# Kernel optimization log

Hardware: AMD Instinct MI355X
Metric: run time of the kernel (lower is better)

## Reference

```python
import jax, jax.numpy as jnp
import numpy as np

P = 65536          # collocation points
J = 16             # num_subdomains == pou num_partitions
WID = 64           # subnet width_size
N_SUB_HID = 2      # subnet depth=3 -> 2 extra hidden linear layers after the input layer
H = 64             # pou hidden_dim
N_POU_RES = 4      # pou depth=6 -> 4 residual blocks


def setup_inputs() -> dict:
    key = jax.random.key(0)
    ks = jax.random.split(key, 14)
    s = 0.1  # small init scale for stable tanh/softmax
    return {
        "x": jax.random.uniform(ks[0], (P, 2), jnp.float32),
        "sub_W0": s * jax.random.normal(ks[1], (J, 2, WID), jnp.float32),
        "sub_b0": s * jax.random.normal(ks[2], (J, WID), jnp.float32),
        "sub_Wh": s * jax.random.normal(ks[3], (J, N_SUB_HID, WID, WID), jnp.float32),
        "sub_bh": s * jax.random.normal(ks[4], (J, N_SUB_HID, WID), jnp.float32),
        "sub_Wl": s * jax.random.normal(ks[5], (J, WID, 1), jnp.float32),
        "sub_bl": s * jax.random.normal(ks[6], (J, 1), jnp.float32),
        "pou_W0": s * jax.random.normal(ks[7], (2, H), jnp.float32),
        "pou_b0": s * jax.random.normal(ks[8], (H,), jnp.float32),
        "pou_Wh": s * jax.random.normal(ks[9], (N_POU_RES, H, H), jnp.float32),
        "pou_bh": s * jax.random.normal(ks[10], (N_POU_RES, H), jnp.float32),
        "pou_Wl": s * jax.random.normal(ks[11], (H, J), jnp.float32),
        "pou_bl": s * jax.random.normal(ks[12], (J,), jnp.float32),
    }


def reference(x, sub_W0, sub_b0, sub_Wh, sub_bh, sub_Wl, sub_bl,
              pou_W0, pou_b0, pou_Wh, pou_bh, pou_Wl, pou_bl):
    x = jnp.atleast_2d(x)
    # --- ResPOUNet2D.forward: partition-of-unity weights (computed ONCE, not per j) ---
    h = jax.nn.relu(x @ pou_W0 + pou_b0)                      # [P, H]
    for i in range(pou_Wh.shape[0]):                          # residual relu blocks
        h = h + jax.nn.relu(h @ pou_Wh[i] + pou_bh[i])
    w_all = jax.nn.softmax(h @ pou_Wl + pou_bl, axis=-1)      # [P, J]
    # --- batched subnets: eqx.nn.MLP with tanh, applied to (x-0.5)*2 ---
    xs = (x - 0.5) * 2.0                                      # [P, 2]
    hs = jnp.tanh(jnp.einsum('pd,jdw->jpw', xs, sub_W0) + sub_b0[:, None, :])  # [J, P, W]
    for i in range(sub_Wh.shape[1]):
        hs = jnp.tanh(jnp.einsum('jpw,jwv->jpv', hs, sub_Wh[:, i]) + sub_bh[:, i][:, None, :])
    u = (jnp.einsum('jpw,jwo->jpo', hs, sub_Wl) + sub_bl[:, None, :])[..., 0]  # [J, P]
    # --- weighted sum over subdomains ---
    total = jnp.einsum('pj,jp->p', w_all, u)                  # [P]
    # --- ansatz: hard zero-Dirichlet BC on unit square ---
    return total * jnp.sin(jnp.pi * x[:, 0]) * jnp.sin(jnp.pi * x[:, 1])
```

## Files before the change

kernel.cpp:

```cpp
#include <hip/hip_runtime.h>
#include <math.h>

#define NP 65536
#define NJ 16
#define WID 64
#define HH 64
#define NPOU 4
#define NSUB 2
#define L2E2 2.8853900817779268f

typedef __attribute__((ext_vector_type(8))) short short8;
typedef __attribute__((ext_vector_type(4))) float f32x4;
typedef __attribute__((ext_vector_type(4))) int int4v;

#define CHUNK_US(row, chunk) ((((row) << 6)) + ((((chunk) ^ ((row) & 7))) << 3))
__device__ __forceinline__ int usIdx(int row, int col) {
    return ((row) << 6) + ((((col >> 3) ^ (row & 7))) << 3) + (col & 7);
}

__device__ __forceinline__ unsigned short f2bf(float f) {
    unsigned u = __float_as_uint(f);
    u += 0x7FFFu + ((u >> 16) & 1u);
    return (unsigned short)(u >> 16);
}
__device__ __forceinline__ unsigned short rhu(float f) {
    return (unsigned short)((__float_as_uint(f) + 0x8000u) >> 16);
}
__device__ __forceinline__ unsigned pk2(float a, float b) {
    unsigned ua = __float_as_uint(a) + 0x8000u;
    unsigned ub = __float_as_uint(b) + 0x8000u;
    return __builtin_amdgcn_perm(ub, ua, 0x07060302u);
}
__device__ __forceinline__ unsigned cvtpk(float a, float b) {
    unsigned r;
    asm("v_cvt_pk_bf16_f32 %0, %1, %2" : "=v"(r) : "v"(a), "v"(b));
    return r;
}
__device__ __forceinline__ float bf2f(unsigned short s) {
    return __uint_as_float(((unsigned)s) << 16);
}
__device__ __forceinline__ float tanh2(float y) {
    float e = __builtin_amdgcn_exp2f(y);
    return fmaf(-2.0f, __builtin_amdgcn_rcpf(e + 1.0f), 1.0f);
}
__device__ __forceinline__ short8 mk8(unsigned a, unsigned b, unsigned c, unsigned d) {
    int4v t; t.x = (int)a; t.y = (int)b; t.z = (int)c; t.w = (int)d;
    return __builtin_bit_cast(short8, t);
}

__global__ __launch_bounds__(256) void pou_mfma_kernel(
    const float* __restrict__ x,
    const float* __restrict__ W0, const float* __restrict__ b0,
    const float* __restrict__ Wh, const float* __restrict__ bh,
    const float* __restrict__ Wl, const float* __restrict__ bl,
    float* __restrict__ w_all)
{
    __shared__ unsigned short sA[4 * 64 * 64];
    __shared__ unsigned short sWhT[NPOU * 64 * 64];
    __shared__ unsigned short sWlT[16 * 64];
    __shared__ float sW0a[HH], sW0b[HH], sB0[HH];
    __shared__ float sbh[NPOU * HH];
    __shared__ float sbl[NJ];

    const int tid  = threadIdx.x;
    const int wave = tid >> 6;
    const int lane = tid & 63;
    const int r15  = lane & 15;
    const int g    = lane >> 4;

    for (int idx = tid; idx < NPOU * HH * HH; idx += 256) {
        int r = idx >> 12, k = (idx >> 6) & 63, n = idx & 63;
        sWhT[r * 4096 + usIdx(n, k)] = f2bf(Wh[idx]);
    }
    for (int idx = tid; idx < HH * NJ; idx += 256) {
        int k = idx >> 4, j = idx & 15;
        sWlT[usIdx(j, k)] = f2bf(Wl[idx]);
    }
    if (tid < HH) { sW0a[tid] = W0[tid]; sW0b[tid] = W0[HH + tid]; sB0[tid] = b0[tid]; }
    for (int i = tid; i < NPOU * HH; i += 256) sbh[i] = bh[i];
    if (tid < NJ) sbl[tid] = bl[tid];
    __syncthreads();

    unsigned short* myA = &sA[wave * 4096];
    const int pbase = blockIdx.x * 256;

    {
        const int p = pbase + tid;
        float2 xv = ((const float2*)x)[p];
        float v[HH];
#pragma unroll
        for (int c = 0; c < HH; ++c)
            v[c] = fmaxf(fmaf(xv.x, sW0a[c], fmaf(xv.y, sW0b[c], sB0[c])), 0.0f);
#pragma unroll
        for (int c = 0; c < 8; ++c) {
            int4v r;
            r.x = (int)pk2(v[8 * c + 0], v[8 * c + 1]);
            r.y = (int)pk2(v[8 * c + 2], v[8 * c + 3]);
            r.z = (int)pk2(v[8 * c + 4], v[8 * c + 5]);
            r.w = (int)pk2(v[8 * c + 6], v[8 * c + 7]);
            *(int4v*)&myA[CHUNK_US(lane, c)] = r;
        }
    }

    float trunk[4][4][4];
#pragma unroll
    for (int mt = 0; mt < 4; ++mt)
#pragma unroll
        for (int nt = 0; nt < 4; ++nt)
#pragma unroll
            for (int q = 0; q < 4; ++q)
                trunk[mt][nt][q] = bf2f(myA[usIdx(mt * 16 + g * 4 + q, nt * 16 + r15)]);

#pragma unroll 1
    for (int r = 0; r < NPOU; ++r) {
        const unsigned short* wt = &sWhT[r * 4096];
        short8 bfr[2][4];
#pragma unroll
        for (int kc = 0; kc < 2; ++kc)
#pragma unroll
            for (int nt = 0; nt < 4; ++nt)
                bfr[kc][nt] = *(const short8*)&wt[CHUNK_US(nt * 16 + r15, kc * 4 + g)];
        float bias[4];
#pragma unroll
        for (int nt = 0; nt < 4; ++nt) bias[nt] = sbh[r * HH + nt * 16 + r15];

#pragma unroll
        for (int mt = 0; mt < 4; ++mt) {
            short8 a0 = *(const short8*)&myA[CHUNK_US(mt * 16 + r15, g)];
            short8 a1 = *(const short8*)&myA[CHUNK_US(mt * 16 + r15, 4 + g)];
            f32x4 acc[4];
#pragma unroll
            for (int nt = 0; nt < 4; ++nt) {
                acc[nt] = (f32x4)(0.0f);
                acc[nt] = __builtin_amdgcn_mfma_f32_16x16x32_bf16(a0, bfr[0][nt], acc[nt], 0, 0, 0);
                acc[nt] = __builtin_amdgcn_mfma_f32_16x16x32_bf16(a1, bfr[1][nt], acc[nt], 0, 0, 0);
            }
#pragma unroll
            for (int nt = 0; nt < 4; ++nt)
#pragma unroll
                for (int q = 0; q < 4; ++q) {
                    float t = trunk[mt][nt][q] + fmaxf(acc[nt][q] + bias[nt], 0.0f);
                    trunk[mt][nt][q] = t;
                    myA[usIdx(mt * 16 + g * 4 + q, nt * 16 + r15)] = rhu(t);
                }
        }
    }

    short8 bw0 = *(const short8*)&sWlT[CHUNK_US(r15, g)];
    short8 bw1 = *(const short8*)&sWlT[CHUNK_US(r15, 4 + g)];
    float lg[4][4], mx[4][4];
#pragma unroll
    for (int mt = 0; mt < 4; ++mt) {
        short8 a0 = *(const short8*)&myA[CHUNK_US(mt * 16 + r15, g)];
        short8 a1 = *(const short8*)&myA[CHUNK_US(mt * 16 + r15, 4 + g)];
        f32x4 acc = (f32x4)(0.0f);
        acc = __builtin_amdgcn_mfma_f32_16x16x32_bf16(a0, bw0, acc, 0, 0, 0);
        acc = __builtin_amdgcn_mfma_f32_16x16x32_bf16(a1, bw1, acc, 0, 0, 0);
#pragma unroll
        for (int q = 0; q < 4; ++q) { lg[mt][q] = acc[q] + sbl[r15]; mx[mt][q] = lg[mt][q]; }
    }
#pragma unroll
    for (int mask = 1; mask < 16; mask <<= 1)
#pragma unroll
        for (int mt = 0; mt < 4; ++mt)
#pragma unroll
            for (int q = 0; q < 4; ++q) mx[mt][q] = fmaxf(mx[mt][q], __shfl_xor(mx[mt][q], mask));
    float ev[4][4], sm[4][4];
#pragma unroll
    for (int mt = 0; mt < 4; ++mt)
#pragma unroll
        for (int q = 0; q < 4; ++q) { ev[mt][q] = __expf(lg[mt][q] - mx[mt][q]); sm[mt][q] = ev[mt][q]; }
#pragma unroll
    for (int mask = 1; mask < 16; mask <<= 1)
#pragma unroll
        for (int mt = 0; mt < 4; ++mt)
#pragma unroll
            for (int q = 0; q < 4; ++q) sm[mt][q] += __shfl_xor(sm[mt][q], mask);
#pragma unroll
    for (int mt = 0; mt < 4; ++mt)
#pragma unroll
        for (int q = 0; q < 4; ++q) {
            const int p = pbase + wave * 64 + mt * 16 + g * 4 + q;
            w_all[r15 * NP + p] = ev[mt][q] * __builtin_amdgcn_rcpf(sm[mt][q]);
        }
}

__global__ __launch_bounds__(256) void prep_kernel(
    const float* __restrict__ gW0, const float* __restrict__ gb0,
    const float* __restrict__ gWh, const float* __restrict__ gbh,
    const float* __restrict__ gWl, const float* __restrict__ gbl,
    int4v* __restrict__ wfrag, float* __restrict__ prm)
{
    const int j   = blockIdx.y;
    const int tid = threadIdx.x;
    const int f   = blockIdx.x * 256 + tid;
    const int lane = f & 63, kc = (f >> 6) & 1, mt = (f >> 7) & 3, L = f >> 9;
    const int c = lane & 15, g = lane >> 4;
    const int n = mt * 16 + c;

    const float* src = gWh + j * (NSUB * WID * WID) + L * 4096;
    unsigned w[4];
#pragma unroll
    for (int e2 = 0; e2 < 4; ++e2) {
        int k = kc * 32 + 8 * g + 2 * e2;
        float v0 = L2E2 * src[k * 64 + n];
        float v1 = L2E2 * src[(k + 1) * 64 + n];
        w[e2] = (unsigned)f2bf(v0) | ((unsigned)f2bf(v1) << 16);
    }
    int4v r; r.x = (int)w[0]; r.y = (int)w[1]; r.z = (int)w[2]; r.w = (int)w[3];
    wfrag[j * 1024 + f] = r;

    if (blockIdx.x == 0) {
        float* pj = prm + j * 512;
        if (tid < WID) {
            float w0 = gW0[j * 2 * WID + tid], w1 = gW0[j * 2 * WID + WID + tid];
            pj[tid]       = 2.0f * L2E2 * w0;
            pj[64 + tid]  = 2.0f * L2E2 * w1;
            pj[128 + tid] = L2E2 * (gb0[j * WID + tid] - w0 - w1);
        }
        if (tid < NSUB * WID) pj[192 + tid] = L2E2 * gbh[j * NSUB * WID + tid];
        if (tid < WID) pj[320 + tid] = gWl[j * WID + tid];
        if (tid == 0) pj[384] = gbl[j];
    }
}

__global__ __launch_bounds__(256, 4) void subnet_nolds_kernel(
    const float* __restrict__ x,
    const short8* __restrict__ wfrag,
    const float* __restrict__ prm,
    const float* __restrict__ w_all,
    float* __restrict__ upart)
{
    const int tid  = threadIdx.x;
    const int j    = blockIdx.y;
    const int wave = tid >> 6;
    const int lane = tid & 63;
    const int c    = lane & 15;
    const int g    = lane >> 4;

    const float*  pj = prm + j * 512;
    const short8* wf = wfrag + j * 1024;
    const int pb = blockIdx.x * 256 + wave * 64;

    short8 bf[2][4];
    {
        float xs0[4], xs1[4];
#pragma unroll
        for (int nt = 0; nt < 4; ++nt) {
            float2 xv = ((const float2*)x)[pb + nt * 16 + c];
            xs0[nt] = xv.x; xs1[nt] = xv.y;
        }
        f32x4 wa[2][2], wb[2][2], bb[2][2];
#pragma unroll
        for (int kc = 0; kc < 2; ++kc)
#pragma unroll
            for (int hf = 0; hf < 2; ++hf) {
                wa[kc][hf] = *(const f32x4*)&pj[      kc * 32 + 8 * g + 4 * hf];
                wb[kc][hf] = *(const f32x4*)&pj[ 64 + kc * 32 + 8 * g + 4 * hf];
                bb[kc][hf] = *(const f32x4*)&pj[128 + kc * 32 + 8 * g + 4 * hf];
            }
        unsigned t[2][4][4];
#pragma unroll
        for (int kc = 0; kc < 2; ++kc)
#pragma unroll
            for (int pr = 0; pr < 4; ++pr) {
                const int h0 = pr >> 1, e0 = (2 * pr) & 3, e1 = e0 + 1;
#pragma unroll
                for (int nt = 0; nt < 4; ++nt) {
                    float v0 = tanh2(fmaf(xs0[nt], wa[kc][h0][e0], fmaf(xs1[nt], wb[kc][h0][e0], bb[kc][h0][e0])));
                    float v1 = tanh2(fmaf(xs0[nt], wa[kc][h0][e1], fmaf(xs1[nt], wb[kc][h0][e1], bb[kc][h0][e1])));
                    t[kc][nt][pr] = cvtpk(v0, v1);
                }
            }
#pragma unroll
        for (int kc = 0; kc < 2; ++kc)
#pragma unroll
            for (int nt = 0; nt < 4; ++nt)
                bf[kc][nt] = mk8(t[kc][nt][0], t[kc][nt][1], t[kc][nt][2], t[kc][nt][3]);
    }

    float red[4];
#pragma unroll
    for (int nt = 0; nt < 4; ++nt) red[nt] = 0.0f;

#pragma unroll
    for (int L = 0; L < NSUB; ++L) {
        short8 aw[4][2];
#pragma unroll
        for (int mt = 0; mt < 4; ++mt)
#pragma unroll
            for (int kc = 0; kc < 2; ++kc)
                aw[mt][kc] = wf[((L * 4 + mt) * 2 + kc) * 64 + lane];
        f32x4 bias[4];
#pragma unroll
        for (int mt = 0; mt < 4; ++mt)
            bias[mt] = *(const f32x4*)&pj[192 + L * 64 + mt * 16 + 4 * g];

#pragma unroll
        for (int nt = 0; nt < 4; ++nt) {
            f32x4 acc[4];
#pragma unroll
            for (int mt = 0; mt < 4; ++mt) acc[mt] = bias[mt];
#pragma unroll
            for (int mt = 0; mt < 4; ++mt) {
                acc[mt] = __builtin_amdgcn_mfma_f32_16x16x32_bf16(aw[mt][0], bf[0][nt], acc[mt], 0, 0, 0);
                acc[mt] = __builtin_amdgcn_mfma_f32_16x16x32_bf16(aw[mt][1], bf[1][nt], acc[mt], 0, 0, 0);
            }

            if (L < NSUB - 1) {
                float h[4][4];
#pragma unroll
                for (int mt = 0; mt < 4; ++mt)
#pragma unroll
                    for (int q = 0; q < 4; ++q) h[mt][q] = tanh2(acc[mt][q]);
#pragma unroll
                for (int kn = 0; kn < 2; ++kn) {
                    unsigned A0 = cvtpk(h[2 * kn][0],     h[2 * kn][1]);
                    unsigned A1 = cvtpk(h[2 * kn][2],     h[2 * kn][3]);
                    unsigned B0 = cvtpk(h[2 * kn + 1][0], h[2 * kn + 1][1]);
                    unsigned B1 = cvtpk(h[2 * kn + 1][2], h[2 * kn + 1][3]);
                    asm("v_permlane32_swap_b32 %0, %1" : "+v"(A0), "+v"(B0));
                    asm("v_permlane16_swap_b32 %0, %1" : "+v"(A0), "+v"(B0));
                    asm("v_permlane32_swap_b32 %0, %1" : "+v"(A1), "+v"(B1));
                    asm("v_permlane16_swap_b32 %0, %1" : "+v"(A1), "+v"(B1));
                    bf[kn][nt] = mk8(A0, A1, B0, B1);
                }
            } else {
#pragma unroll
                for (int mt = 0; mt < 4; ++mt) {
                    f32x4 wlv = *(const f32x4*)&pj[320 + mt * 16 + 4 * g];
#pragma unroll
                    for (int q = 0; q < 4; ++q)
                        red[nt] = fmaf(tanh2(acc[mt][q]), wlv[q], red[nt]);
                }
            }
        }
    }

#pragma unroll
    for (int nt = 0; nt < 4; ++nt) {
        red[nt] += __shfl_xor(red[nt], 16);
        red[nt] += __shfl_xor(red[nt], 32);
    }
    float u = (g & 1) ? ((g & 2) ? red[3] : red[1]) : ((g & 2) ? red[2] : red[0]);
    u += pj[384];

    const int p = pb + lane;
    upart[j * NP + p] = u * w_all[j * NP + p];
}

__global__ __launch_bounds__(256) void subnet_mfma_fallback(
    const float* __restrict__ x,
    const float* __restrict__ gW0, const float* __restrict__ gb0,
    const float* __restrict__ gWh, const float* __restrict__ gbh,
    const float* __restrict__ gWl, const float* __restrict__ gbl,
    const float* __restrict__ w_all,
    float* __restrict__ upart)
{
    __shared__ __align__(16) unsigned short sWt[NSUB * 64 * 64];
    __shared__ __align__(16) float sW0a[WID], sW0b[WID], sB0[WID];
    __shared__ __align__(16) float sbh[NSUB * WID];
    __shared__ __align__(16) float sWl[WID];
    __shared__ float sbl1v;

    const int tid  = threadIdx.x;
    const int j    = blockIdx.y;
    const int wave = tid >> 6;
    const int lane = tid & 63;
    const int c    = lane & 15;
    const int g    = lane >> 4;

    {
        const float* src = gWh + j * (NSUB * WID * WID);
        for (int idx = tid; idx < NSUB * WID * WID; idx += 256) {
            int L = idx >> 12, rem = idx & 4095;
            int k = rem >> 6, n = rem & 63;
            sWt[L * 4096 + usIdx(n, k)] = f2bf(L2E2 * src[idx]);
        }
        if (tid < WID) {
            float w0 = gW0[j * 2 * WID + tid], w1 = gW0[j * 2 * WID + WID + tid];
            sW0a[tid] = 2.0f * L2E2 * w0;
            sW0b[tid] = 2.0f * L2E2 * w1;
            sB0[tid]  = L2E2 * (gb0[j * WID + tid] - w0 - w1);
        }
        if (tid < NSUB * WID) sbh[tid] = L2E2 * gbh[j * NSUB * WID + tid];
        if (tid < WID) sWl[tid] = gWl[j * WID + tid];
        if (tid == 0) sbl1v = gbl[j];
    }
    __syncthreads();

    const int pb = blockIdx.x * 256 + wave * 64;

    short8 bf[2][4];
    {
        float xs0[4], xs1[4];
#pragma unroll
        for (int nt = 0; nt < 4; ++nt) {
            float2 xv = ((const float2*)x)[pb + nt * 16 + c];
            xs0[nt] = xv.x; xs1[nt] = xv.y;
        }
        f32x4 wa[2][2], wb[2][2], bb[2][2];
#pragma unroll
        for (int kc = 0; kc < 2; ++kc)
#pragma unroll
            for (int hf = 0; hf < 2; ++hf) {
                wa[kc][hf] = *(const f32x4*)&sW0a[kc * 32 + 8 * g + 4 * hf];
                wb[kc][hf] = *(const f32x4*)&sW0b[kc * 32 + 8 * g + 4 * hf];
                bb[kc][hf] = *(const f32x4*)&sB0 [kc * 32 + 8 * g + 4 * hf];
            }
        unsigned t[2][4][4];
#pragma unroll
        for (int kc = 0; kc < 2; ++kc)
#pragma unroll
            for (int pr = 0; pr < 4; ++pr) {
                const int h0 = pr >> 1, e0 = (2 * pr) & 3, e1 = e0 + 1;
#pragma unroll
                for (int nt = 0; nt < 4; ++nt) {
                    float v0 = tanh2(fmaf(xs0[nt], wa[kc][h0][e0], fmaf(xs1[nt], wb[kc][h0][e0], bb[kc][h0][e0])));
                    float v1 = tanh2(fmaf(xs0[nt], wa[kc][h0][e1], fmaf(xs1[nt], wb[kc][h0][e1], bb[kc][h0][e1])));
                    t[kc][nt][pr] = cvtpk(v0, v1);
                }
            }
#pragma unroll
        for (int kc = 0; kc < 2; ++kc)
#pragma unroll
            for (int nt = 0; nt < 4; ++nt)
                bf[kc][nt] = mk8(t[kc][nt][0], t[kc][nt][1], t[kc][nt][2], t[kc][nt][3]);
    }

    float red[4];
#pragma unroll
    for (int nt = 0; nt < 4; ++nt) red[nt] = 0.0f;

#pragma unroll
    for (int L = 0; L < NSUB; ++L) {
        const unsigned short* wt = &sWt[L * 4096];
        short8 aw[4][2];
#pragma unroll
        for (int mt = 0; mt < 4; ++mt)
#pragma unroll
            for (int kc = 0; kc < 2; ++kc)
                aw[mt][kc] = *(const short8*)&wt[CHUNK_US(mt * 16 + c, kc * 4 + g)];
        f32x4 bias[4];
#pragma unroll
        for (int mt = 0; mt < 4; ++mt)
            bias[mt] = *(const f32x4*)&sbh[L * 64 + mt * 16 + 4 * g];

#pragma unroll
        for (int nt = 0; nt < 4; ++nt) {
            f32x4 acc[4];
#pragma unroll
            for (int mt = 0; mt < 4; ++mt) acc[mt] = bias[mt];
#pragma unroll
            for (int mt = 0; mt < 4; ++mt) {
                acc[mt] = __builtin_amdgcn_mfma_f32_16x16x32_bf16(aw[mt][0], bf[0][nt], acc[mt], 0, 0, 0);
                acc[mt] = __builtin_amdgcn_mfma_f32_16x16x32_bf16(aw[mt][1], bf[1][nt], acc[mt], 0, 0, 0);
            }

            if (L < NSUB - 1) {
                float h[4][4];
#pragma unroll
                for (int mt = 0; mt < 4; ++mt)
#pragma unroll
                    for (int q = 0; q < 4; ++q) h[mt][q] = tanh2(acc[mt][q]);
#pragma unroll
                for (int kn = 0; kn < 2; ++kn) {
                    unsigned A0 = cvtpk(h[2 * kn][0],     h[2 * kn][1]);
                    unsigned A1 = cvtpk(h[2 * kn][2],     h[2 * kn][3]);
                    unsigned B0 = cvtpk(h[2 * kn + 1][0], h[2 * kn + 1][1]);
                    unsigned B1 = cvtpk(h[2 * kn + 1][2], h[2 * kn + 1][3]);
                    asm("v_permlane32_swap_b32 %0, %1" : "+v"(A0), "+v"(B0));
                    asm("v_permlane16_swap_b32 %0, %1" : "+v"(A0), "+v"(B0));
                    asm("v_permlane32_swap_b32 %0, %1" : "+v"(A1), "+v"(B1));
                    asm("v_permlane16_swap_b32 %0, %1" : "+v"(A1), "+v"(B1));
                    bf[kn][nt] = mk8(A0, A1, B0, B1);
                }
            } else {
#pragma unroll
                for (int mt = 0; mt < 4; ++mt) {
                    f32x4 wlv = *(const f32x4*)&sWl[mt * 16 + 4 * g];
#pragma unroll
                    for (int q = 0; q < 4; ++q)
                        red[nt] = fmaf(tanh2(acc[mt][q]), wlv[q], red[nt]);
                }
            }
        }
    }

#pragma unroll
    for (int nt = 0; nt < 4; ++nt) {
        red[nt] += __shfl_xor(red[nt], 16);
        red[nt] += __shfl_xor(red[nt], 32);
    }
    float u = (g & 1) ? ((g & 2) ? red[3] : red[1]) : ((g & 2) ? red[2] : red[0]);
    u += sbl1v;

    const int p = pb + lane;
    upart[j * NP + p] = u * w_all[j * NP + p];
}

__global__ __launch_bounds__(256) void reduce_kernel(
    const float* __restrict__ x,
    const float* __restrict__ upart,
    float* __restrict__ out)
{
    const int p4 = blockIdx.x * 256 + threadIdx.x;
    f32x4 s = (f32x4)(0.0f);
#pragma unroll
    for (int j = 0; j < NJ; ++j) s += *(const f32x4*)&upart[j * NP + 4 * p4];
    f32x4 xa = ((const f32x4*)x)[2 * p4];
    f32x4 xb = ((const f32x4*)x)[2 * p4 + 1];
    f32x4 o;
    o.x = s.x * __builtin_amdgcn_sinf(xa.x * 0.5f) * __builtin_amdgcn_sinf(xa.y * 0.5f);
    o.y = s.y * __builtin_amdgcn_sinf(xa.z * 0.5f) * __builtin_amdgcn_sinf(xa.w * 0.5f);
    o.z = s.z * __builtin_amdgcn_sinf(xb.x * 0.5f) * __builtin_amdgcn_sinf(xb.y * 0.5f);
    o.w = s.w * __builtin_amdgcn_sinf(xb.z * 0.5f) * __builtin_amdgcn_sinf(xb.w * 0.5f);
    *(f32x4*)&out[4 * p4] = o;
}

extern "C" void kernel_launch(void* const* d_in, const int* in_sizes, int n_in,
                              void* d_out, int out_size, void* d_ws, size_t ws_size,
                              hipStream_t stream) {
    const float* x      = (const float*)d_in[0];
    const float* sub_W0 = (const float*)d_in[1];
    const float* sub_b0 = (const float*)d_in[2];
    const float* sub_Wh = (const float*)d_in[3];
    const float* sub_bh = (const float*)d_in[4];
    const float* sub_Wl = (const float*)d_in[5];
    const float* sub_bl = (const float*)d_in[6];
    const float* pou_W0 = (const float*)d_in[7];
    const float* pou_b0 = (const float*)d_in[8];
    const float* pou_Wh = (const float*)d_in[9];
    const float* pou_bh = (const float*)d_in[10];
    const float* pou_Wl = (const float*)d_in[11];
    const float* pou_bl = (const float*)d_in[12];

    float* w_all = (float*)d_ws;
    float* upart = (float*)d_ws + (size_t)NJ * NP;
    char*  extra = (char*)d_ws + (size_t)2 * NJ * NP * 4;
    void*  wfrag = (void*)extra;
    float* prm   = (float*)(extra + (size_t)NJ * 1024 * 16);

    const size_t need = (size_t)2 * NJ * NP * 4 + (size_t)NJ * 1024 * 16 + (size_t)NJ * 512 * 4;
    const bool use_prep = (ws_size >= need);

    pou_mfma_kernel<<<NP / 256, 256, 0, stream>>>(x, pou_W0, pou_b0, pou_Wh, pou_bh,
                                                  pou_Wl, pou_bl, w_all);

    if (use_prep) {
        dim3 gp(4, NJ);
        prep_kernel<<<gp, 256, 0, stream>>>(sub_W0, sub_b0, sub_Wh, sub_bh, sub_Wl, sub_bl,
                                            (int4v*)wfrag, prm);
        dim3 g2(NP / 256, NJ);
        subnet_nolds_kernel<<<g2, 256, 0, stream>>>(x, (const short8*)wfrag, prm, w_all, upart);
    } else {
        dim3 g2(NP / 256, NJ);
        subnet_mfma_fallback<<<g2, 256, 0, stream>>>(x, sub_W0, sub_b0, sub_Wh, sub_bh,
                                                     sub_Wl, sub_bl, w_all, upart);
    }

    reduce_kernel<<<NP / 1024, 256, 0, stream>>>(x, upart, (float*)d_out);
}
```

Baseline: 72.96 us.

## Shrink per-wave tile to 16 points in POU and subnet kernels

Replaces the LDS-staged POU kernel and the 64-points-per-wave subnet kernel with variants that handle 16 points per wave. Weights come in as prepacked bf16 MFMA fragments read straight from global memory, built by a new POU prep kernel. The aim is to cut register pressure and per-wave serial MFMA chains, raise the number of waves in flight, and drop LDS staging from the POU network. In exchange every fragment load is repeated per 16 points rather than reused across four point tiles, so global and L2 weight traffic grows, and there is one extra launch.

After: 99.40 us. 1.36x slower.

```diff
diff --git a/kernel.cpp b/kernel.cpp
--- a/kernel.cpp
+++ b/kernel.cpp
@@ -46,6 +46,252 @@
 __device__ __forceinline__ short8 mk8(unsigned a, unsigned b, unsigned c, unsigned d) {
     int4v t; t.x = (int)a; t.y = (int)b; t.z = (int)c; t.w = (int)d;
     return __builtin_bit_cast(short8, t);
+}
+#define CB_TRANSFORM(hsrc, bfdst)                                              \
+    {                                                                          \
+        _Pragma("unroll")                                                      \
+        for (int kn = 0; kn < 2; ++kn) {                                       \
+            unsigned A0 = cvtpk(hsrc[2 * kn][0],     hsrc[2 * kn][1]);         \
+            unsigned A1 = cvtpk(hsrc[2 * kn][2],     hsrc[2 * kn][3]);         \
+            unsigned B0 = cvtpk(hsrc[2 * kn + 1][0], hsrc[2 * kn + 1][1]);     \
+            unsigned B1 = cvtpk(hsrc[2 * kn + 1][2], hsrc[2 * kn + 1][3]);     \
+            asm("v_permlane32_swap_b32 %0, %1" : "+v"(A0), "+v"(B0));          \
+            asm("v_permlane16_swap_b32 %0, %1" : "+v"(A0), "+v"(B0));          \
+            asm("v_permlane32_swap_b32 %0, %1" : "+v"(A1), "+v"(B1));          \
+            asm("v_permlane16_swap_b32 %0, %1" : "+v"(A1), "+v"(B1));          \
+            bfdst[kn] = mk8(A0, A1, B0, B1);                                   \
+        }                                                                      \
+    }
+
+__global__ __launch_bounds__(256) void prep_kernel(
+    const float* __restrict__ gW0, const float* __restrict__ gb0,
+    const float* __restrict__ gWh, const float* __restrict__ gbh,
+    const float* __restrict__ gWl, const float* __restrict__ gbl,
+    int4v* __restrict__ wfrag, float* __restrict__ prm)
+{
+    const int j   = blockIdx.y;
+    const int tid = threadIdx.x;
+    const int f   = blockIdx.x * 256 + tid;
+    const int lane = f & 63, kc = (f >> 6) & 1, mt = (f >> 7) & 3, L = f >> 9;
+    const int c = lane & 15, g = lane >> 4;
+    const int n = mt * 16 + c;
+
+    const float* src = gWh + j * (NSUB * WID * WID) + L * 4096;
+    unsigned w[4];
+#pragma unroll
+    for (int e2 = 0; e2 < 4; ++e2) {
+        int k = kc * 32 + 8 * g + 2 * e2;
+        float v0 = L2E2 * src[k * 64 + n];
+        float v1 = L2E2 * src[(k + 1) * 64 + n];
+        w[e2] = (unsigned)f2bf(v0) | ((unsigned)f2bf(v1) << 16);
+    }
+    int4v r; r.x = (int)w[0]; r.y = (int)w[1]; r.z = (int)w[2]; r.w = (int)w[3];
+    wfrag[j * 1024 + f] = r;
+
+    if (blockIdx.x == 0) {
+        float* pj = prm + j * 512;
+        if (tid < WID) {
+            float w0 = gW0[j * 2 * WID + tid], w1 = gW0[j * 2 * WID + WID + tid];
+            pj[tid]       = 2.0f * L2E2 * w0;
+            pj[64 + tid]  = 2.0f * L2E2 * w1;
+            pj[128 + tid] = L2E2 * (gb0[j * WID + tid] - w0 - w1);
+        }
+        if (tid < NSUB * WID) pj[192 + tid] = L2E2 * gbh[j * NSUB * WID + tid];
+        if (tid < WID) pj[320 + tid] = gWl[j * WID + tid];
+        if (tid == 0) pj[384] = gbl[j];
+    }
+}
+
+__global__ __launch_bounds__(256) void prep_pou_kernel(
+    const float* __restrict__ W0, const float* __restrict__ b0,
+    const float* __restrict__ Wh, const float* __restrict__ bh,
+    const float* __restrict__ Wl, const float* __restrict__ bl,
+    int4v* __restrict__ pwf, float* __restrict__ pp)
+{
+    const int tid = threadIdx.x;
+    const int idx = blockIdx.x * 256 + tid;
+
+    if (idx < 2048) {
+        const int r = idx >> 9, mt = (idx >> 7) & 3, kc = (idx >> 6) & 1, lane = idx & 63;
+        const int c = lane & 15, g = lane >> 4;
+        const int n = mt * 16 + c;
+        const float* src = Wh + r * 4096;
+        unsigned w[4];
+#pragma unroll
+        for (int e2 = 0; e2 < 4; ++e2) {
+            int k = kc * 32 + 8 * g + 2 * e2;
+            w[e2] = (unsigned)f2bf(src[k * 64 + n]) | ((unsigned)f2bf(src[(k + 1) * 64 + n]) << 16);
+        }
+        int4v rr; rr.x = (int)w[0]; rr.y = (int)w[1]; rr.z = (int)w[2]; rr.w = (int)w[3];
+        pwf[idx] = rr;
+    } else if (idx < 2176) {
+        const int t = idx - 2048;
+        const int kc = t >> 6, lane = t & 63;
+        const int jj = lane & 15, g = lane >> 4;
+        unsigned w[4];
+#pragma unroll
+        for (int e2 = 0; e2 < 4; ++e2) {
+            int k = kc * 32 + 8 * g + 2 * e2;
+            w[e2] = (unsigned)f2bf(Wl[k * 16 + jj]) | ((unsigned)f2bf(Wl[(k + 1) * 16 + jj]) << 16);
+        }
+        int4v rr; rr.x = (int)w[0]; rr.y = (int)w[1]; rr.z = (int)w[2]; rr.w = (int)w[3];
+        pwf[idx] = rr;
+    }
+    if (blockIdx.x == 8) {
+        if (tid < HH) {
+            pp[tid]       = W0[tid];
+            pp[64 + tid]  = W0[HH + tid];
+            pp[128 + tid] = b0[tid];
+        }
+        pp[192 + tid] = bh[tid];
+        if (tid < NJ) pp[448 + tid] = bl[tid];
+    }
+}
+
+__global__ __launch_bounds__(256) void pou16_kernel(
+    const float* __restrict__ x,
+    const short8* __restrict__ pwf, const float* __restrict__ pp,
+    float* __restrict__ w_all)
+{
+    const int tid = threadIdx.x, wave = tid >> 6, lane = tid & 63;
+    const int c = lane & 15, g = lane >> 4;
+    const int pb = blockIdx.x * 64 + wave * 16;
+
+    float2 xv = ((const float2*)x)[pb + c];
+
+    float trunk[4][4];
+#pragma unroll
+    for (int mt = 0; mt < 4; ++mt) {
+        f32x4 a  = *(const f32x4*)&pp[      mt * 16 + 4 * g];
+        f32x4 b  = *(const f32x4*)&pp[ 64 + mt * 16 + 4 * g];
+        f32x4 bb = *(const f32x4*)&pp[128 + mt * 16 + 4 * g];
+#pragma unroll
+        for (int q = 0; q < 4; ++q)
+            trunk[mt][q] = fmaxf(fmaf(xv.x, a[q], fmaf(xv.y, b[q], bb[q])), 0.0f);
+    }
+
+#pragma unroll
+    for (int r = 0; r < NPOU; ++r) {
+        short8 bf[2];
+        CB_TRANSFORM(trunk, bf);
+        f32x4 acc[4];
+#pragma unroll
+        for (int mt = 0; mt < 4; ++mt)
+            acc[mt] = *(const f32x4*)&pp[192 + r * 64 + mt * 16 + 4 * g];
+#pragma unroll
+        for (int mt = 0; mt < 4; ++mt) {
+            short8 a0 = pwf[((r * 4 + mt) * 2 + 0) * 64 + lane];
+            short8 a1 = pwf[((r * 4 + mt) * 2 + 1) * 64 + lane];
+            acc[mt] = __builtin_amdgcn_mfma_f32_16x16x32_bf16(a0, bf[0], acc[mt], 0, 0, 0);
+            acc[mt] = __builtin_amdgcn_mfma_f32_16x16x32_bf16(a1, bf[1], acc[mt], 0, 0, 0);
+        }
+#pragma unroll
+        for (int mt = 0; mt < 4; ++mt)
+#pragma unroll
+            for (int q = 0; q < 4; ++q)
+                trunk[mt][q] += fmaxf(acc[mt][q], 0.0f);
+    }
+
+    short8 bfl[2];
+    CB_TRANSFORM(trunk, bfl);
+    f32x4 lac = *(const f32x4*)&pp[448 + 4 * g];
+    lac = __builtin_amdgcn_mfma_f32_16x16x32_bf16(pwf[2048 + lane],      bfl[0], lac, 0, 0, 0);
+    lac = __builtin_amdgcn_mfma_f32_16x16x32_bf16(pwf[2048 + 64 + lane], bfl[1], lac, 0, 0, 0);
+
+    float m = fmaxf(fmaxf(lac[0], lac[1]), fmaxf(lac[2], lac[3]));
+    m = fmaxf(m, __shfl_xor(m, 16));
+    m = fmaxf(m, __shfl_xor(m, 32));
+    float ev[4]; float s = 0.0f;
+#pragma unroll
+    for (int q = 0; q < 4; ++q) { ev[q] = __expf(lac[q] - m); s += ev[q]; }
+    s += __shfl_xor(s, 16);
+    s += __shfl_xor(s, 32);
+    const float rinv = __builtin_amdgcn_rcpf(s);
+#pragma unroll
+    for (int q = 0; q < 4; ++q)
+        w_all[(4 * g + q) * NP + pb + c] = ev[q] * rinv;
+}
+
+__global__ __launch_bounds__(256) void subnet16_kernel(
+    const float* __restrict__ x,
+    const short8* __restrict__ wfrag,
+    const float* __restrict__ prm,
+    const float* __restrict__ w_all,
+    float* __restrict__ upart)
+{
+    const int tid = threadIdx.x;
+    const int j   = blockIdx.y;
+    const int wave = tid >> 6, lane = tid & 63;
+    const int c = lane & 15, g = lane >> 4;
+
+    const float*  pj = prm + j * 512;
+    const short8* wf = wfrag + j * 1024;
+    const int pb = blockIdx.x * 64 + wave * 16;
+
+    float2 xv = ((const float2*)x)[pb + c];
+
+    short8 bf[2];
+#pragma unroll
+    for (int kc = 0; kc < 2; ++kc) {
+        f32x4 wa[2], wb[2], bb[2];
+#pragma unroll
+        for (int hf = 0; hf < 2; ++hf) {
+            wa[hf] = *(const f32x4*)&pj[      kc * 32 + 8 * g + 4 * hf];
+            wb[hf] = *(const f32x4*)&pj[ 64 + kc * 32 + 8 * g + 4 * hf];
+            bb[hf] = *(const f32x4*)&pj[128 + kc * 32 + 8 * g + 4 * hf];
+        }
+        unsigned t[4];
+#pragma unroll
+        for (int pr = 0; pr < 4; ++pr) {
+            const int h0 = pr >> 1, e0 = (2 * pr) & 3, e1 = e0 + 1;
+            float v0 = tanh2(fmaf(xv.x, wa[h0][e0], fmaf(xv.y, wb[h0][e0], bb[h0][e0])));
+            float v1 = tanh2(fmaf(xv.x, wa[h0][e1], fmaf(xv.y, wb[h0][e1], bb[h0][e1])));
+            t[pr] = cvtpk(v0, v1);
+        }
+        bf[kc] = mk8(t[0], t[1], t[2], t[3]);
+    }
+
+    float red = 0.0f;
+
+#pragma unroll
+    for (int L = 0; L < NSUB; ++L) {
+        f32x4 acc[4];
+#pragma unroll
+        for (int mt = 0; mt < 4; ++mt)
+            acc[mt] = *(const f32x4*)&pj[192 + L * 64 + mt * 16 + 4 * g];
+#pragma unroll
+        for (int mt = 0; mt < 4; ++mt) {
+            short8 a0 = wf[((L * 4 + mt) * 2 + 0) * 64 + lane];
+            short8 a1 = wf[((L * 4 + mt) * 2 + 1) * 64 + lane];
+            acc[mt] = __builtin_amdgcn_mfma_f32_16x16x32_bf16(a0, bf[0], acc[mt], 0, 0, 0);
+            acc[mt] = __builtin_amdgcn_mfma_f32_16x16x32_bf16(a1, bf[1], acc[mt], 0, 0, 0);
+        }
+
+        if (L < NSUB - 1) {
+            float h[4][4];
+#pragma unroll
+            for (int mt = 0; mt < 4; ++mt)
+#pragma unroll
+                for (int q = 0; q < 4; ++q) h[mt][q] = tanh2(acc[mt][q]);
+            CB_TRANSFORM(h, bf);
+        } else {
+#pragma unroll
+            for (int mt = 0; mt < 4; ++mt) {
+                f32x4 wlv = *(const f32x4*)&pj[320 + mt * 16 + 4 * g];
+#pragma unroll
+                for (int q = 0; q < 4; ++q)
+                    red = fmaf(tanh2(acc[mt][q]), wlv[q], red);
+            }
+        }
+    }
+
+    red += __shfl_xor(red, 16);
+    red += __shfl_xor(red, 32);
+    if (g == 0) {
+        const int p = pb + c;
+        float u = red + pj[384];
+        upart[j * NP + p] = u * w_all[j * NP + p];
+    }
 }
 
 __global__ __launch_bounds__(256) void pou_mfma_kernel(
@@ -185,170 +431,6 @@
         }
 }
 
-__global__ __launch_bounds__(256) void prep_kernel(
-    const float* __restrict__ gW0, const float* __restrict__ gb0,
-    const float* __restrict__ gWh, const float* __restrict__ gbh,
-    const float* __restrict__ gWl, const float* __restrict__ gbl,
-    int4v* __restrict__ wfrag, float* __restrict__ prm)
-{
-    const int j   = blockIdx.y;
-    const int tid = threadIdx.x;
-    const int f   = blockIdx.x * 256 + tid;
-    const int lane = f & 63, kc = (f >> 6) & 1, mt = (f >> 7) & 3, L = f >> 9;
-    const int c = lane & 15, g = lane >> 4;
-    const int n = mt * 16 + c;
-
-    const float* src = gWh + j * (NSUB * WID * WID) + L * 4096;
-    unsigned w[4];
-#pragma unroll
-    for (int e2 = 0; e2 < 4; ++e2) {
-        int k = kc * 32 + 8 * g + 2 * e2;
-        float v0 = L2E2 * src[k * 64 + n];
-        float v1 = L2E2 * src[(k + 1) * 64 + n];
-        w[e2] = (unsigned)f2bf(v0) | ((unsigned)f2bf(v1) << 16);
-    }
-    int4v r; r.x = (int)w[0]; r.y = (int)w[1]; r.z = (int)w[2]; r.w = (int)w[3];
-    wfrag[j * 1024 + f] = r;
-
-    if (blockIdx.x == 0) {
-        float* pj = prm + j * 512;
-        if (tid < WID) {
-            float w0 = gW0[j * 2 * WID + tid], w1 = gW0[j * 2 * WID + WID + tid];
-            pj[tid]       = 2.0f * L2E2 * w0;
-            pj[64 + tid]  = 2.0f * L2E2 * w1;
-            pj[128 + tid] = L2E2 * (gb0[j * WID + tid] - w0 - w1);
-        }
-        if (tid < NSUB * WID) pj[192 + tid] = L2E2 * gbh[j * NSUB * WID + tid];
-        if (tid < WID) pj[320 + tid] = gWl[j * WID + tid];
-        if (tid == 0) pj[384] = gbl[j];
-    }
-}
-
-__global__ __launch_bounds__(256, 4) void subnet_nolds_kernel(
-    const float* __restrict__ x,
-    const short8* __restrict__ wfrag,
-    const float* __restrict__ prm,
-    const float* __restrict__ w_all,
-    float* __restrict__ upart)
-{
-    const int tid  = threadIdx.x;
-    const int j    = blockIdx.y;
-    const int wave = tid >> 6;
-    const int lane = tid & 63;
-    const int c    = lane & 15;
-    const int g    = lane >> 4;
-
-    const float*  pj = prm + j * 512;
-    const short8* wf = wfrag + j * 1024;
-    const int pb = blockIdx.x * 256 + wave * 64;
-
-    short8 bf[2][4];
-    {
-        float xs0[4], xs1[4];
-#pragma unroll
-        for (int nt = 0; nt < 4; ++nt) {
-            float2 xv = ((const float2*)x)[pb + nt * 16 + c];
-            xs0[nt] = xv.x; xs1[nt] = xv.y;
-        }
-        f32x4 wa[2][2], wb[2][2], bb[2][2];
-#pragma unroll
-        for (int kc = 0; kc < 2; ++kc)
-#pragma unroll
-            for (int hf = 0; hf < 2; ++hf) {
-                wa[kc][hf] = *(const f32x4*)&pj[      kc * 32 + 8 * g + 4 * hf];
-                wb[kc][hf] = *(const f32x4*)&pj[ 64 + kc * 32 + 8 * g + 4 * hf];
-                bb[kc][hf] = *(const f32x4*)&pj[128 + kc * 32 + 8 * g + 4 * hf];
-            }
-        unsigned t[2][4][4];
-#pragma unroll
-        for (int kc = 0; kc < 2; ++kc)
-#pragma unroll
-            for (int pr = 0; pr < 4; ++pr) {
-                const int h0 = pr >> 1, e0 = (2 * pr) & 3, e1 = e0 + 1;
-#pragma unroll
-                for (int nt = 0; nt < 4; ++nt) {
-                    float v0 = tanh2(fmaf(xs0[nt], wa[kc][h0][e0], fmaf(xs1[nt], wb[kc][h0][e0], bb[kc][h0][e0])));
-                    float v1 = tanh2(fmaf(xs0[nt], wa[kc][h0][e1], fmaf(xs1[nt], wb[kc][h0][e1], bb[kc][h0][e1])));
-                    t[kc][nt][pr] = cvtpk(v0, v1);
-                }
-            }
-#pragma unroll
-        for (int kc = 0; kc < 2; ++kc)
-#pragma unroll
-            for (int nt = 0; nt < 4; ++nt)
-                bf[kc][nt] = mk8(t[kc][nt][0], t[kc][nt][1], t[kc][nt][2], t[kc][nt][3]);
-    }
-
-    float red[4];
-#pragma unroll
-    for (int nt = 0; nt < 4; ++nt) red[nt] = 0.0f;
-
-#pragma unroll
-    for (int L = 0; L < NSUB; ++L) {
-        short8 aw[4][2];
-#pragma unroll
-        for (int mt = 0; mt < 4; ++mt)
-#pragma unroll
-            for (int kc = 0; kc < 2; ++kc)
-                aw[mt][kc] = wf[((L * 4 + mt) * 2 + kc) * 64 + lane];
-        f32x4 bias[4];
-#pragma unroll
-        for (int mt = 0; mt < 4; ++mt)
-            bias[mt] = *(const f32x4*)&pj[192 + L * 64 + mt * 16 + 4 * g];
-
-#pragma unroll
-        for (int nt = 0; nt < 4; ++nt) {
-            f32x4 acc[4];
-#pragma unroll
-            for (int mt = 0; mt < 4; ++mt) acc[mt] = bias[mt];
-#pragma unroll
-            for (int mt = 0; mt < 4; ++mt) {
-                acc[mt] = __builtin_amdgcn_mfma_f32_16x16x32_bf16(aw[mt][0], bf[0][nt], acc[mt], 0, 0, 0);
-                acc[mt] = __builtin_amdgcn_mfma_f32_16x16x32_bf16(aw[mt][1], bf[1][nt], acc[mt], 0, 0, 0);
-            }
-
-            if (L < NSUB - 1) {
-                float h[4][4];
-#pragma unroll
-                for (int mt = 0; mt < 4; ++mt)
-#pragma unroll
-                    for (int q = 0; q < 4; ++q) h[mt][q] = tanh2(acc[mt][q]);
-#pragma unroll
-                for (int kn = 0; kn < 2; ++kn) {
-                    unsigned A0 = cvtpk(h[2 * kn][0],     h[2 * kn][1]);
-                    unsigned A1 = cvtpk(h[2 * kn][2],     h[2 * kn][3]);
-                    unsigned B0 = cvtpk(h[2 * kn + 1][0], h[2 * kn + 1][1]);
-                    unsigned B1 = cvtpk(h[2 * kn + 1][2], h[2 * kn + 1][3]);
-                    asm("v_permlane32_swap_b32 %0, %1" : "+v"(A0), "+v"(B0));
-                    asm("v_permlane16_swap_b32 %0, %1" : "+v"(A0), "+v"(B0));
-                    asm("v_permlane32_swap_b32 %0, %1" : "+v"(A1), "+v"(B1));
-                    asm("v_permlane16_swap_b32 %0, %1" : "+v"(A1), "+v"(B1));
-                    bf[kn][nt] = mk8(A0, A1, B0, B1);
-                }
-            } else {
-#pragma unroll
-                for (int mt = 0; mt < 4; ++mt) {
-                    f32x4 wlv = *(const f32x4*)&pj[320 + mt * 16 + 4 * g];
-#pragma unroll
-                    for (int q = 0; q < 4; ++q)
-                        red[nt] = fmaf(tanh2(acc[mt][q]), wlv[q], red[nt]);
-                }
-            }
-        }
-    }
-
-#pragma unroll
-    for (int nt = 0; nt < 4; ++nt) {
-        red[nt] += __shfl_xor(red[nt], 16);
-        red[nt] += __shfl_xor(red[nt], 32);
-    }
-    float u = (g & 1) ? ((g & 2) ? red[3] : red[1]) : ((g & 2) ? red[2] : red[0]);
-    u += pj[384];
-
-    const int p = pb + lane;
-    upart[j * NP + p] = u * w_all[j * NP + p];
-}
-
 __global__ __launch_bounds__(256) void subnet_mfma_fallback(
     const float* __restrict__ x,
     const float* __restrict__ gW0, const float* __restrict__ gb0,
@@ -463,18 +545,10 @@
                 for (int mt = 0; mt < 4; ++mt)
 #pragma unroll
                     for (int q = 0; q < 4; ++q) h[mt][q] = tanh2(acc[mt][q]);
-#pragma unroll
-                for (int kn = 0; kn < 2; ++kn) {
-                    unsigned A0 = cvtpk(h[2 * kn][0],     h[2 * kn][1]);
-                    unsigned A1 = cvtpk(h[2 * kn][2],     h[2 * kn][3]);
-                    unsigned B0 = cvtpk(h[2 * kn + 1][0], h[2 * kn + 1][1]);
-                    unsigned B1 = cvtpk(h[2 * kn + 1][2], h[2 * kn + 1][3]);
-                    asm("v_permlane32_swap_b32 %0, %1" : "+v"(A0), "+v"(B0));
-                    asm("v_permlane16_swap_b32 %0, %1" : "+v"(A0), "+v"(B0));
-                    asm("v_permlane32_swap_b32 %0, %1" : "+v"(A1), "+v"(B1));
-                    asm("v_permlane16_swap_b32 %0, %1" : "+v"(A1), "+v"(B1));
-                    bf[kn][nt] = mk8(A0, A1, B0, B1);
-                }
+                short8 btmp[2];
+                CB_TRANSFORM(h, btmp);
+                bf[0][nt] = btmp[0];
+                bf[1][nt] = btmp[1];
             } else {
 #pragma unroll
                 for (int mt = 0; mt < 4; ++mt) {
@@ -537,23 +611,29 @@
 
     float* w_all = (float*)d_ws;
     float* upart = (float*)d_ws + (size_t)NJ * NP;
-    char*  extra = (char*)d_ws + (size_t)2 * NJ * NP * 4;
-    void*  wfrag = (void*)extra;
-    float* prm   = (float*)(extra + (size_t)NJ * 1024 * 16);
-
-    const size_t need = (size_t)2 * NJ * NP * 4 + (size_t)NJ * 1024 * 16 + (size_t)NJ * 512 * 4;
+    char*  extra  = (char*)d_ws + (size_t)2 * NJ * NP * 4;
+    void*  swf    = (void*)extra;
+    float* sprm   = (float*)(extra + (size_t)NJ * 1024 * 16);
+    char*  extra2 = extra + (size_t)NJ * 1024 * 16 + (size_t)NJ * 512 * 4;
+    void*  pwf    = (void*)extra2;
+    float* pprm   = (float*)(extra2 + 2176 * 16);
+
+    const size_t need = (size_t)2 * NJ * NP * 4 + (size_t)NJ * 1024 * 16
+                      + (size_t)NJ * 512 * 4 + 2176 * 16 + 512 * 4;
     const bool use_prep = (ws_size >= need);
-
-    pou_mfma_kernel<<<NP / 256, 256, 0, stream>>>(x, pou_W0, pou_b0, pou_Wh, pou_bh,
-                                                  pou_Wl, pou_bl, w_all);
 
     if (use_prep) {
         dim3 gp(4, NJ);
         prep_kernel<<<gp, 256, 0, stream>>>(sub_W0, sub_b0, sub_Wh, sub_bh, sub_Wl, sub_bl,
-                                            (int4v*)wfrag, prm);
-        dim3 g2(NP / 256, NJ);
-        subnet_nolds_kernel<<<g2, 256, 0, stream>>>(x, (const short8*)wfrag, prm, w_all, upart);
+                                            (int4v*)swf, sprm);
+        prep_pou_kernel<<<9, 256, 0, stream>>>(pou_W0, pou_b0, pou_Wh, pou_bh, pou_Wl, pou_bl,
+                                               (int4v*)pwf, pprm);
+        pou16_kernel<<<NP / 64, 256, 0, stream>>>(x, (const short8*)pwf, pprm, w_all);
+        dim3 g2(NP / 64, NJ);
+        subnet16_kernel<<<g2, 256, 0, stream>>>(x, (const short8*)swf, sprm, w_all, upart);
     } else {
+        pou_mfma_kernel<<<NP / 256, 256, 0, stream>>>(x, pou_W0, pou_b0, pou_Wh, pou_bh,
+                                                      pou_Wl, pou_bl, w_all);
         dim3 g2(NP / 256, NJ);
         subnet_mfma_fallback<<<g2, 256, 0, stream>>>(x, sub_W0, sub_b0, sub_Wh, sub_bh,
                                                      sub_Wl, sub_bl, w_all, upart);
```
